# Kernel tuning notes

Hardware: AMD Instinct MI355X
Metric: run time of the kernel (lower is better)

Reference implementation:

```python
import jax, jax.numpy as jnp
import numpy as np

TOP_K = 2
NUM_EXPERTS = 16
CAPACITY = 512          # >> avg load (128/expert) so no token is ever dropped in practice
FP8_MAX = 448.0         # float8_e4m3fn max representable magnitude


def _fp8_quant(v, axes):
    """Simulated fp8 e4m3 dynamic quantization: amax scaling + clipping.
    Returns (quantized values, scale with keepdims)."""
    s = jnp.clip(jnp.max(jnp.abs(v), axis=axes, keepdims=True) / FP8_MAX, 1e-12, None)
    return jnp.clip(v / s, -FP8_MAX, FP8_MAX), s


def setup_inputs() -> dict:
    key = jax.random.key(0)
    k0, k1, k2, k3 = jax.random.split(key, 4)
    T, H, I, E = 1024, 2048, 1408, NUM_EXPERTS
    x = jax.random.normal(k0, (T, H), jnp.float32)
    router_logits = jax.random.normal(k1, (T, E), jnp.float32)
    w13_weight = jax.random.normal(k2, (E, 2 * I, H), jnp.float32) * 0.02
    w2_weight = jax.random.normal(k3, (E, H, I), jnp.float32) * 0.02
    return {"x": x, "router_logits": router_logits,
            "w13_weight": w13_weight, "w2_weight": w2_weight}


def reference(x, router_logits, w13_weight, w2_weight):
    T, H = x.shape
    E, K, C = NUM_EXPERTS, TOP_K, CAPACITY
    I = w2_weight.shape[2]

    # --- routing: softmax -> top-k -> renormalize ---
    probs = jax.nn.softmax(router_logits, axis=-1)               # [T, E]
    topw, topi = jax.lax.top_k(probs, K)                          # [T, K]
    topw = topw / jnp.sum(topw, axis=-1, keepdims=True)

    # --- dispatch: flatten (token, k) rows, rank within expert ---
    rid = topi.reshape(-1)                                        # [T*K] expert id per row
    rtok = jnp.arange(T * K) // K                                 # source token per row
    order = jnp.argsort(rid)                                      # jax sort is stable
    counts = jnp.bincount(rid, length=E)
    offsets = jnp.concatenate([jnp.zeros(1, counts.dtype), jnp.cumsum(counts)[:-1]])
    pos_sorted = jnp.arange(T * K) - offsets[rid[order]]
    pos = jnp.zeros(T * K, jnp.int32).at[order].set(pos_sorted.astype(jnp.int32))
    valid = pos < C                                               # capacity is generous: no drops
    posc = jnp.minimum(pos, C - 1)

    xrows = x[rtok] * valid[:, None].astype(x.dtype)              # [T*K, H]
    xbuf = jnp.zeros((E, C, H), x.dtype).at[rid, posc].add(xrows)  # [E, C, H]

    # --- grouped GEMM 1 (gate+up), fp8 w8a8: per-expert weight scale, per-token act scale ---
    w13q, sw13 = _fp8_quant(w13_weight, (1, 2))                   # sw13 [E,1,1]
    xq, sa1 = _fp8_quant(xbuf, -1)                                # sa1  [E,C,1]
    h = jnp.einsum('ech,efh->ecf', xq, w13q) * (sa1 * sw13)       # [E, C, 2I]

    # --- silu_and_mul ---
    gate, up = h[..., :I], h[..., I:]
    act = jax.nn.silu(gate) * up                                  # [E, C, I]

    # --- grouped GEMM 2 (down) ---
    w2q, sw2 = _fp8_quant(w2_weight, (1, 2))                      # sw2 [E,1,1]
    aq, sa2 = _fp8_quant(act, -1)                                 # sa2 [E,C,1]
    ybuf = jnp.einsum('eci,ehi->ech', aq, w2q) * (sa2 * sw2)      # [E, C, H]

    # --- combine: gather back and weight by router probs ---
    yrows = ybuf[rid, posc] * valid[:, None].astype(x.dtype)      # [T*K, H]
    out = jnp.einsum('tkh,tk->th', yrows.reshape(T, K, H), topw)  # [T, H]
    return out
```

## Files before the change

### kernel.cpp

```cpp
#include <hip/hip_runtime.h>
#include <hip/hip_bf16.h>
#include <math.h>

#define NEXP 16
#define CAP  512
#define TTOK 1024
#define HDIM 2048
#define IDIM 1408
#define MAXR (TTOK*2)

typedef float fx4 __attribute__((ext_vector_type(4)));
typedef short short8 __attribute__((ext_vector_type(8)));
typedef unsigned int u32;
typedef unsigned long long u64;

__device__ __forceinline__ unsigned short f2bf(float f) {
    u32 u = __float_as_uint(f);
    u += 0x7FFFu + ((u >> 16) & 1u);
    return (unsigned short)(u >> 16);
}
__device__ __forceinline__ u64 pack4bf(fx4 f) {
    u32 lo = (u32)f2bf(f.x) | ((u32)f2bf(f.y) << 16);
    u32 hi = (u32)f2bf(f.z) | ((u32)f2bf(f.w) << 16);
    return (u64)lo | ((u64)hi << 32);
}

__global__ void router_kernel(const float* __restrict__ logits,
                              int* __restrict__ topi, float* __restrict__ topw,
                              int* __restrict__ cnt1) {
    int t = blockIdx.x * blockDim.x + threadIdx.x;
    if (t >= TTOK) return;
    const float* l = logits + t * NEXP;
    float b0 = -INFINITY, b1 = -INFINITY; int i0 = 0, i1 = 0;
    for (int e = 0; e < NEXP; ++e) {
        float v = l[e];
        if (v > b0) { b1 = b0; i1 = i0; b0 = v; i0 = e; }
        else if (v > b1) { b1 = v; i1 = e; }
    }
    float w0 = 1.f / (1.f + expf(b1 - b0));
    topi[t*2]   = i0; topi[t*2+1] = i1;
    topw[t*2]   = w0; topw[t*2+1] = 1.f - w0;
    atomicAdd(&cnt1[i0], 1);
    atomicAdd(&cnt1[i1], 1);
}

__global__ void scan_kernel(const int* __restrict__ cnt1, int* __restrict__ base) {
    if (threadIdx.x == 0 && blockIdx.x == 0) {
        int s = 0;
        for (int e = 0; e < NEXP; ++e) {
            base[e] = s;
            int c = cnt1[e]; if (c > CAP) c = CAP;
            s += c;
        }
        base[NEXP] = s;
    }
}

__global__ void assign_kernel(const int* __restrict__ topi, const int* __restrict__ base,
                              int* __restrict__ cnt2,
                              int* __restrict__ slot_token, int* __restrict__ slot_of) {
    int t = blockIdx.x * blockDim.x + threadIdx.x;
    if (t >= TTOK) return;
    for (int k = 0; k < 2; ++k) {
        int e = topi[t*2+k];
        int p = atomicAdd(&cnt2[e], 1);
        if (p < CAP) {
            int s = base[e] + p;
            slot_token[s] = t;
            slot_of[t*2+k] = s;
        } else {
            slot_of[t*2+k] = -1;
        }
    }
}

__global__ void gather_kernel(const float* __restrict__ x,
                              const int* __restrict__ slot_token,
                              const int* __restrict__ base,
                              unsigned short* __restrict__ A1) {
    int s = blockIdx.x;
    if (s >= base[NEXP]) return;
    int t = slot_token[s];
    int c = threadIdx.x * 8;
    const float* src = x + (size_t)t * HDIM + c;
    fx4 a = *(const fx4*)src, b = *(const fx4*)(src + 4);
    u64 v[2] = { pack4bf(a), pack4bf(b) };
    *(fx4*)&A1[(size_t)s * HDIM + c] = *(fx4*)v;
}

#define LDA 40

template<int NDIM, int KDIM, int SK>
__global__ __launch_bounds__(256) void gemm_bt_kernel(
    const unsigned short* __restrict__ A,
    const float* __restrict__ W,
    float* __restrict__ Cpart,
    const int* __restrict__ base)
{
    const int e = blockIdx.z;
    const int n0 = base[e];
    const int rows = base[e+1] - n0;
    const int ks = blockIdx.y % SK;
    const int rtile = (blockIdx.y / SK) * 128;
    if (rtile >= rows) return;
    const int col0 = blockIdx.x * 64;
    const int kbase = ks * (KDIM / SK);

    __shared__ unsigned short sA[2][128 * LDA];
    __shared__ unsigned short sB[2][64 * LDA];

    const int tid = threadIdx.x;
    const int lane = tid & 63;
    const int wv = tid >> 6;
    const int lr = lane & 15;
    const int quad = lane >> 4;

    fx4 acc[2][4];
    #pragma unroll
    for (int i = 0; i < 2; ++i)
        #pragma unroll
        for (int j = 0; j < 4; ++j) acc[i][j] = (fx4)0.f;

    const int ag = tid & 3, ar = tid >> 2;
    const int bg = tid & 3, bc = tid >> 2;

    int arow[2];
    #pragma unroll
    for (int p = 0; p < 2; ++p) {
        int grow = rtile + ar + p*64;
        arow[p] = (grow < rows) ? (n0 + grow) : -1;
    }

    const float* Wp = W + ((size_t)e * NDIM + col0) * KDIM + kbase;
    const unsigned short* Ap = A + kbase;

    fx4 pa[2][2], pb[2][2];

    auto prefetch = [&](int slot, int k0) {
        #pragma unroll
        for (int p = 0; p < 2; ++p)
            pb[slot][p] = *(const fx4*)(Wp + (size_t)bc * KDIM + k0 + (bg + p*4)*4);
        #pragma unroll
        for (int p = 0; p < 2; ++p)
            pa[slot][p] = (arow[p] >= 0)
                ? *(const fx4*)(Ap + (size_t)arow[p]*KDIM + k0 + ag*8)
                : (fx4)0.f;
    };
    auto stage = [&](int buf, int slot) {
        #pragma unroll
        for (int p = 0; p < 2; ++p)
            *(u64*)&sB[buf][bc*LDA + (bg + p*4)*4] = pack4bf(pb[slot][p]);
        #pragma unroll
        for (int p = 0; p < 2; ++p)
            *(fx4*)&sA[buf][(ar + p*64)*LDA + ag*8] = pa[slot][p];
    };

    const int KT = (KDIM / SK) / 32;
    prefetch(0, 0);
    stage(0, 0);
    if (KT > 1) prefetch(1, 32);
    __syncthreads();

    for (int kt = 0; kt < KT; ++kt) {
        const int cur = kt & 1;
        if (kt + 2 < KT) prefetch(cur, (kt + 2) * 32);

        short8 af[2], bfr[4];
        #pragma unroll
        for (int mi = 0; mi < 2; ++mi)
            af[mi] = *(const short8*)&sA[cur][(wv*32 + mi*16 + lr)*LDA + quad*8];
        #pragma unroll
        for (int ni = 0; ni < 4; ++ni)
            bfr[ni] = *(const short8*)&sB[cur][(ni*16 + lr)*LDA + quad*8];
        #pragma unroll
        for (int mi = 0; mi < 2; ++mi)
            #pragma unroll
            for (int ni = 0; ni < 4; ++ni)
                acc[mi][ni] = __builtin_amdgcn_mfma_f32_16x16x32_bf16(
                    af[mi], bfr[ni], acc[mi][ni], 0, 0, 0);

        if (kt + 1 < KT) {
            stage(1 - cur, 1 - cur);
            __syncthreads();
        }
    }

    float* Cp = Cpart + (size_t)ks * MAXR * NDIM;
    #pragma unroll
    for (int mi = 0; mi < 2; ++mi) {
        #pragma unroll
        for (int r = 0; r < 4; ++r) {
            int grow = rtile + wv*32 + mi*16 + quad*4 + r;
            if (grow < rows) {
                size_t orow = (size_t)(n0 + grow) * NDIM;
                #pragma unroll
                for (int ni = 0; ni < 4; ++ni) {
                    int gcol = col0 + ni*16 + lr;
                    Cp[orow + gcol] = acc[mi][ni][r];
                }
            }
        }
    }
}

__global__ void silu_kernel(const float* __restrict__ h,
                            unsigned short* __restrict__ act,
                            const int* __restrict__ base) {
    const int R = base[NEXP];
    int idx = blockIdx.x * blockDim.x + threadIdx.x;
    int row = idx / (IDIM/8);
    int j   = idx % (IDIM/8);
    if (row >= R) return;
    const float* g0 = h + (size_t)row * (2*IDIM) + j*8;
    const float* g1 = g0 + (size_t)MAXR * (2*IDIM);
    float gate[8], up[8];
    *(fx4*)&gate[0] = *(const fx4*)g0        + *(const fx4*)g1;
    *(fx4*)&gate[4] = *(const fx4*)(g0+4)    + *(const fx4*)(g1+4);
    *(fx4*)&up[0]   = *(const fx4*)(g0+IDIM)   + *(const fx4*)(g1+IDIM);
    *(fx4*)&up[4]   = *(const fx4*)(g0+IDIM+4) + *(const fx4*)(g1+IDIM+4);
    unsigned short ao[8];
    #pragma unroll
    for (int i = 0; i < 8; ++i) {
        float gv = gate[i];
        float s = gv / (1.f + __expf(-gv));
        ao[i] = f2bf(s * up[i]);
    }
    *(fx4*)&act[(size_t)row*IDIM + j*8] = *(fx4*)ao;
}

__global__ void combine_kernel(const float* __restrict__ ypart,
                               const int* __restrict__ slot_of,
                               const float* __restrict__ topw,
                               float* __restrict__ out) {
    int t = blockIdx.x;
    int c = threadIdx.x * 8;
    int s0 = slot_of[t*2], s1 = slot_of[t*2+1];
    float w0 = topw[t*2], w1 = topw[t*2+1];
    const float* y1b = ypart + (size_t)MAXR * HDIM;
    float res[8];
    #pragma unroll
    for (int i = 0; i < 8; ++i) res[i] = 0.f;
    if (s0 >= 0) {
        const float* p0 = ypart + (size_t)s0*HDIM + c;
        const float* p1 = y1b   + (size_t)s0*HDIM + c;
        #pragma unroll
        for (int i = 0; i < 8; ++i) res[i] += w0 * (p0[i] + p1[i]);
    }
    if (s1 >= 0) {
        const float* p0 = ypart + (size_t)s1*HDIM + c;
        const float* p1 = y1b   + (size_t)s1*HDIM + c;
        #pragma unroll
        for (int i = 0; i < 8; ++i) res[i] += w1 * (p0[i] + p1[i]);
    }
    float* o = out + (size_t)t*HDIM + c;
    *(fx4*)o       = *(fx4*)res;
    *(fx4*)(o + 4) = *(fx4*)(res + 4);
}

extern "C" void kernel_launch(void* const* d_in, const int* in_sizes, int n_in,
                              void* d_out, int out_size, void* d_ws, size_t ws_size,
                              hipStream_t stream) {
    const float* x      = (const float*)d_in[0];
    const float* logits = (const float*)d_in[1];
    const float* w13    = (const float*)d_in[2];
    const float* w2     = (const float*)d_in[3];
    float* out = (float*)d_out;

    char* ws = (char*)d_ws;
    size_t off = 0;
    auto alloc = [&](size_t bytes) -> void* {
        void* p = ws + off;
        off += (bytes + 255) & ~(size_t)255;
        return p;
    };
    int*   topi       = (int*)  alloc(TTOK*2*sizeof(int));
    float* topw       = (float*)alloc(TTOK*2*sizeof(float));
    int*   cnt1       = (int*)  alloc(NEXP*sizeof(int));
    int*   cnt2       = (int*)  alloc(NEXP*sizeof(int));
    int*   base       = (int*)  alloc((NEXP+1)*sizeof(int));
    int*   slot_token = (int*)  alloc(TTOK*2*sizeof(int));
    int*   slot_of    = (int*)  alloc(TTOK*2*sizeof(int));
    unsigned short* A1  = (unsigned short*)alloc((size_t)MAXR * HDIM * 2);
    float* hpart = (float*)alloc((size_t)2 * MAXR * (2*IDIM) * sizeof(float));
    unsigned short* act = (unsigned short*)alloc((size_t)MAXR * IDIM * 2);
    float* ypart = (float*)alloc((size_t)2 * MAXR * HDIM * sizeof(float));

    hipMemsetAsync(cnt1, 0, NEXP*sizeof(int), stream);
    hipMemsetAsync(cnt2, 0, NEXP*sizeof(int), stream);

    router_kernel<<<dim3((TTOK+255)/256), 256, 0, stream>>>(logits, topi, topw, cnt1);
    scan_kernel<<<1, 64, 0, stream>>>(cnt1, base);
    assign_kernel<<<dim3((TTOK+255)/256), 256, 0, stream>>>(topi, base, cnt2, slot_token, slot_of);
    gather_kernel<<<dim3(MAXR), 256, 0, stream>>>(x, slot_token, base, A1);

    gemm_bt_kernel<2*IDIM, HDIM, 2>
        <<<dim3(2*IDIM/64, (CAP/128)*2, NEXP), 256, 0, stream>>>(
            A1, w13, hpart, base);

    silu_kernel<<<dim3((TTOK*2*(IDIM/8) + 255)/256), 256, 0, stream>>>(hpart, act, base);

    gemm_bt_kernel<HDIM, IDIM, 2>
        <<<dim3(HDIM/64, (CAP/128)*2, NEXP), 256, 0, stream>>>(
            act, w2, ypart, base);

    combine_kernel<<<dim3(TTOK), 256, 0, stream>>>(ypart, slot_of, topw, out);
}
```

Before: 718.7 us.

## Fuse SiLU into gate/up GEMM epilogue, drop split-K, widen tiles to 128x128

```diff
diff --git a/kernel.cpp b/kernel.cpp
--- a/kernel.cpp
+++ b/kernel.cpp
@@ -1,5 +1,4 @@
 #include <hip/hip_runtime.h>
-#include <hip/hip_bf16.h>
 #include <math.h>
 
 #define NEXP 16
@@ -90,29 +89,30 @@
 
 #define LDA 40
 
-template<int NDIM, int KDIM, int SK>
-__global__ __launch_bounds__(256) void gemm_bt_kernel(
+template<int KDIM, bool FUSE>
+__global__ __launch_bounds__(512, 4) void gemm_fused_kernel(
     const unsigned short* __restrict__ A,
     const float* __restrict__ W,
-    float* __restrict__ Cpart,
+    unsigned short* __restrict__ act_out,
+    float* __restrict__ y_out,
     const int* __restrict__ base)
 {
     const int e = blockIdx.z;
     const int n0 = base[e];
     const int rows = base[e+1] - n0;
-    const int ks = blockIdx.y % SK;
-    const int rtile = (blockIdx.y / SK) * 128;
+    const int rtile = blockIdx.y * 128;
     if (rtile >= rows) return;
-    const int col0 = blockIdx.x * 64;
-    const int kbase = ks * (KDIM / SK);
+    const int bx = blockIdx.x;
 
     __shared__ unsigned short sA[2][128 * LDA];
-    __shared__ unsigned short sB[2][64 * LDA];
-
-    const int tid = threadIdx.x;
+    __shared__ unsigned short sB[2][128 * LDA];
+
+    const int tid  = threadIdx.x;
     const int lane = tid & 63;
-    const int wv = tid >> 6;
-    const int lr = lane & 15;
+    const int wv   = tid >> 6;
+    const int wr   = wv & 3;
+    const int wc   = wv >> 2;
+    const int lr   = lane & 15;
     const int quad = lane >> 4;
 
     fx4 acc[2][4];
@@ -124,54 +124,56 @@
     const int ag = tid & 3, ar = tid >> 2;
     const int bg = tid & 3, bc = tid >> 2;
 
-    int arow[2];
-    #pragma unroll
-    for (int p = 0; p < 2; ++p) {
-        int grow = rtile + ar + p*64;
-        arow[p] = (grow < rows) ? (n0 + grow) : -1;
-    }
-
-    const float* Wp = W + ((size_t)e * NDIM + col0) * KDIM + kbase;
-    const unsigned short* Ap = A + kbase;
-
-    fx4 pa[2][2], pb[2][2];
-
-    auto prefetch = [&](int slot, int k0) {
-        #pragma unroll
-        for (int p = 0; p < 2; ++p)
-            pb[slot][p] = *(const fx4*)(Wp + (size_t)bc * KDIM + k0 + (bg + p*4)*4);
-        #pragma unroll
-        for (int p = 0; p < 2; ++p)
-            pa[slot][p] = (arow[p] >= 0)
-                ? *(const fx4*)(Ap + (size_t)arow[p]*KDIM + k0 + ag*8)
-                : (fx4)0.f;
-    };
-    auto stage = [&](int buf, int slot) {
-        #pragma unroll
-        for (int p = 0; p < 2; ++p)
-            *(u64*)&sB[buf][bc*LDA + (bg + p*4)*4] = pack4bf(pb[slot][p]);
-        #pragma unroll
-        for (int p = 0; p < 2; ++p)
-            *(fx4*)&sA[buf][(ar + p*64)*LDA + ag*8] = pa[slot][p];
-    };
-
-    const int KT = (KDIM / SK) / 32;
-    prefetch(0, 0);
-    stage(0, 0);
-    if (KT > 1) prefetch(1, 32);
+    const int agrow = rtile + ar;
+    const bool aval = (agrow < rows);
+    const unsigned short* Ap = A + (size_t)(aval ? (n0 + agrow) : n0) * KDIM + ag * 8;
+
+    int brow;
+    if (FUSE) brow = (bc < 64) ? (bx*64 + bc) : (IDIM + bx*64 + (bc - 64));
+    else      brow = bx*128 + bc;
+    const int NW = FUSE ? (2*IDIM) : HDIM;
+    const float* Wp = W + ((size_t)e * NW + brow) * KDIM + bg * 8;
+
+    fx4 pa[2];
+    fx4 pb[4][2];
+
+    auto prefA = [&](int s, int k0) {
+        pa[s] = aval ? *(const fx4*)(Ap + k0) : (fx4)0.f;
+    };
+    auto prefB = [&](int s, int k0) {
+        pb[s][0] = *(const fx4*)(Wp + k0);
+        pb[s][1] = *(const fx4*)(Wp + k0 + 4);
+    };
+    auto stage = [&](int buf, int sa, int sb) {
+        u64 v[2] = { pack4bf(pb[sb][0]), pack4bf(pb[sb][1]) };
+        *(fx4*)&sB[buf][bc * LDA + bg * 8] = *(fx4*)v;
+        *(fx4*)&sA[buf][ar * LDA + ag * 8] = pa[sa];
+    };
+
+    const int KT = KDIM / 32;
+
+    prefA(0, 0);  prefB(0, 0);
+    stage(0, 0, 0);
+    prefA(1, 32);
+    prefB(1, 32); prefB(2, 64); prefB(3, 96);
     __syncthreads();
 
+    #pragma unroll 4
     for (int kt = 0; kt < KT; ++kt) {
         const int cur = kt & 1;
-        if (kt + 2 < KT) prefetch(cur, (kt + 2) * 32);
+        if (kt + 2 < KT) prefA(cur,     (kt + 2) * 32);
+        if (kt + 4 < KT) prefB(kt & 3,  (kt + 4) * 32);
 
         short8 af[2], bfr[4];
         #pragma unroll
         for (int mi = 0; mi < 2; ++mi)
-            af[mi] = *(const short8*)&sA[cur][(wv*32 + mi*16 + lr)*LDA + quad*8];
-        #pragma unroll
-        for (int ni = 0; ni < 4; ++ni)
-            bfr[ni] = *(const short8*)&sB[cur][(ni*16 + lr)*LDA + quad*8];
+            af[mi] = *(const short8*)&sA[cur][(wr*32 + mi*16 + lr) * LDA + quad*8];
+        #pragma unroll
+        for (int ni = 0; ni < 4; ++ni) {
+            const int rb = FUSE ? ((ni < 2) ? (wc*32 + ni*16) : (64 + wc*32 + (ni-2)*16))
+                                : (wc*64 + ni*16);
+            bfr[ni] = *(const short8*)&sB[cur][(rb + lr) * LDA + quad*8];
+        }
         #pragma unroll
         for (int mi = 0; mi < 2; ++mi)
             #pragma unroll
@@ -180,55 +182,47 @@
                     af[mi], bfr[ni], acc[mi][ni], 0, 0, 0);
 
         if (kt + 1 < KT) {
-            stage(1 - cur, 1 - cur);
+            stage(1 - cur, (kt + 1) & 1, (kt + 1) & 3);
             __syncthreads();
         }
     }
 
-    float* Cp = Cpart + (size_t)ks * MAXR * NDIM;
-    #pragma unroll
-    for (int mi = 0; mi < 2; ++mi) {
-        #pragma unroll
-        for (int r = 0; r < 4; ++r) {
-            int grow = rtile + wv*32 + mi*16 + quad*4 + r;
-            if (grow < rows) {
-                size_t orow = (size_t)(n0 + grow) * NDIM;
+    if (FUSE) {
+        #pragma unroll
+        for (int mi = 0; mi < 2; ++mi) {
+            #pragma unroll
+            for (int nj = 0; nj < 2; ++nj) {
+                const int col = bx*64 + wc*32 + nj*16 + lr;
                 #pragma unroll
-                for (int ni = 0; ni < 4; ++ni) {
-                    int gcol = col0 + ni*16 + lr;
-                    Cp[orow + gcol] = acc[mi][ni][r];
+                for (int r = 0; r < 4; ++r) {
+                    const int gr = rtile + wr*32 + mi*16 + quad*4 + r;
+                    if (gr < rows) {
+                        float g = acc[mi][nj][r];
+                        float u = acc[mi][nj + 2][r];
+                        float s = g / (1.f + __expf(-g)) * u;
+                        act_out[(size_t)(n0 + gr) * IDIM + col] = f2bf(s);
+                    }
                 }
             }
         }
-    }
-}
-
-__global__ void silu_kernel(const float* __restrict__ h,
-                            unsigned short* __restrict__ act,
-                            const int* __restrict__ base) {
-    const int R = base[NEXP];
-    int idx = blockIdx.x * blockDim.x + threadIdx.x;
-    int row = idx / (IDIM/8);
-    int j   = idx % (IDIM/8);
-    if (row >= R) return;
-    const float* g0 = h + (size_t)row * (2*IDIM) + j*8;
-    const float* g1 = g0 + (size_t)MAXR * (2*IDIM);
-    float gate[8], up[8];
-    *(fx4*)&gate[0] = *(const fx4*)g0        + *(const fx4*)g1;
-    *(fx4*)&gate[4] = *(const fx4*)(g0+4)    + *(const fx4*)(g1+4);
-    *(fx4*)&up[0]   = *(const fx4*)(g0+IDIM)   + *(const fx4*)(g1+IDIM);
-    *(fx4*)&up[4]   = *(const fx4*)(g0+IDIM+4) + *(const fx4*)(g1+IDIM+4);
-    unsigned short ao[8];
-    #pragma unroll
-    for (int i = 0; i < 8; ++i) {
-        float gv = gate[i];
-        float s = gv / (1.f + __expf(-gv));
-        ao[i] = f2bf(s * up[i]);
-    }
-    *(fx4*)&act[(size_t)row*IDIM + j*8] = *(fx4*)ao;
-}
-
-__global__ void combine_kernel(const float* __restrict__ ypart,
+    } else {
+        #pragma unroll
+        for (int mi = 0; mi < 2; ++mi) {
+            #pragma unroll
+            for (int ni = 0; ni < 4; ++ni) {
+                const int col = bx*128 + wc*64 + ni*16 + lr;
+                #pragma unroll
+                for (int r = 0; r < 4; ++r) {
+                    const int gr = rtile + wr*32 + mi*16 + quad*4 + r;
+                    if (gr < rows)
+                        y_out[(size_t)(n0 + gr) * HDIM + col] = acc[mi][ni][r];
+                }
+            }
+        }
+    }
+}
+
+__global__ void combine_kernel(const float* __restrict__ y,
                                const int* __restrict__ slot_of,
                                const float* __restrict__ topw,
                                float* __restrict__ out) {
@@ -236,23 +230,20 @@
     int c = threadIdx.x * 8;
     int s0 = slot_of[t*2], s1 = slot_of[t*2+1];
     float w0 = topw[t*2], w1 = topw[t*2+1];
-    const float* y1b = ypart + (size_t)MAXR * HDIM;
     float res[8];
     #pragma unroll
     for (int i = 0; i < 8; ++i) res[i] = 0.f;
     if (s0 >= 0) {
-        const float* p0 = ypart + (size_t)s0*HDIM + c;
-        const float* p1 = y1b   + (size_t)s0*HDIM + c;
-        #pragma unroll
-        for (int i = 0; i < 8; ++i) res[i] += w0 * (p0[i] + p1[i]);
+        const float* p = y + (size_t)s0 * HDIM + c;
+        #pragma unroll
+        for (int i = 0; i < 8; ++i) res[i] += w0 * p[i];
     }
     if (s1 >= 0) {
-        const float* p0 = ypart + (size_t)s1*HDIM + c;
-        const float* p1 = y1b   + (size_t)s1*HDIM + c;
-        #pragma unroll
-        for (int i = 0; i < 8; ++i) res[i] += w1 * (p0[i] + p1[i]);
-    }
-    float* o = out + (size_t)t*HDIM + c;
+        const float* p = y + (size_t)s1 * HDIM + c;
+        #pragma unroll
+        for (int i = 0; i < 8; ++i) res[i] += w1 * p[i];
+    }
+    float* o = out + (size_t)t * HDIM + c;
     *(fx4*)o       = *(fx4*)res;
     *(fx4*)(o + 4) = *(fx4*)(res + 4);
 }
@@ -281,9 +272,8 @@
     int*   slot_token = (int*)  alloc(TTOK*2*sizeof(int));
     int*   slot_of    = (int*)  alloc(TTOK*2*sizeof(int));
     unsigned short* A1  = (unsigned short*)alloc((size_t)MAXR * HDIM * 2);
-    float* hpart = (float*)alloc((size_t)2 * MAXR * (2*IDIM) * sizeof(float));
     unsigned short* act = (unsigned short*)alloc((size_t)MAXR * IDIM * 2);
-    float* ypart = (float*)alloc((size_t)2 * MAXR * HDIM * sizeof(float));
+    float* ybuf = (float*)alloc((size_t)MAXR * HDIM * sizeof(float));
 
     hipMemsetAsync(cnt1, 0, NEXP*sizeof(int), stream);
     hipMemsetAsync(cnt2, 0, NEXP*sizeof(int), stream);
@@ -293,15 +283,11 @@
     assign_kernel<<<dim3((TTOK+255)/256), 256, 0, stream>>>(topi, base, cnt2, slot_token, slot_of);
     gather_kernel<<<dim3(MAXR), 256, 0, stream>>>(x, slot_token, base, A1);
 
-    gemm_bt_kernel<2*IDIM, HDIM, 2>
-        <<<dim3(2*IDIM/64, (CAP/128)*2, NEXP), 256, 0, stream>>>(
-            A1, w13, hpart, base);
-
-    silu_kernel<<<dim3((TTOK*2*(IDIM/8) + 255)/256), 256, 0, stream>>>(hpart, act, base);
-
-    gemm_bt_kernel<HDIM, IDIM, 2>
-        <<<dim3(HDIM/64, (CAP/128)*2, NEXP), 256, 0, stream>>>(
-            act, w2, ypart, base);
-
-    combine_kernel<<<dim3(TTOK), 256, 0, stream>>>(ypart, slot_of, topw, out);
-}
+    gemm_fused_kernel<HDIM, true>
+        <<<dim3(IDIM/64, CAP/128, NEXP), 512, 0, stream>>>(A1, w13, act, nullptr, base);
+
+    gemm_fused_kernel<IDIM, false>
+        <<<dim3(HDIM/128, CAP/128, NEXP), 512, 0, stream>>>(act, w2, nullptr, ybuf, base);
+
+    combine_kernel<<<dim3(TTOK), 256, 0, stream>>>(ybuf, slot_of, topw, out);
+}
```

New measurement: 713.4 us. Within noise of the previous version (-0.7%).
